# Optimization experiments

Hardware: AMD Instinct MI355X
Metric: run time of the kernel (lower is better)

The kernel has to match this reference:

```python
import jax, jax.numpy as jnp
import numpy as np

DIM = 256
NUM_HEADS = 8
WS = 8
HEAD_DIM = DIM // NUM_HEADS
N = WS * WS
B_NW = 8192


def _relative_position_index():
    coords = np.stack(np.meshgrid(np.arange(WS), np.arange(WS), indexing='ij')).reshape(2, -1)  # [2, N]
    rel = coords[:, :, None] - coords[:, None, :]           # [2, N, N]
    rel = rel.transpose(1, 2, 0)                            # [N, N, 2]
    rel[:, :, 0] += WS - 1
    rel[:, :, 1] += WS - 1
    rel[:, :, 0] *= 2 * WS - 1
    return rel.sum(-1).astype(np.int32)                     # [N, N]


def setup_inputs() -> dict:
    key = jax.random.key(0)
    ks = jax.random.split(key, 6)
    x = jax.random.normal(ks[0], (B_NW, N, DIM), dtype=jnp.float32)
    qkv_w = jax.random.normal(ks[1], (3 * DIM, DIM), dtype=jnp.float32) * (DIM ** -0.5)
    qkv_b = jnp.zeros((3 * DIM,), dtype=jnp.float32)
    proj_w = jax.random.normal(ks[2], (DIM, DIM), dtype=jnp.float32) * (DIM ** -0.5)
    proj_b = jnp.zeros((DIM,), dtype=jnp.float32)
    rel_bias_table = jax.random.normal(ks[3], ((2 * WS - 1) ** 2, NUM_HEADS), dtype=jnp.float32) * 0.02
    rel_pos_index = jnp.asarray(_relative_position_index())
    return {"x": x, "qkv_w": qkv_w, "qkv_b": qkv_b, "proj_w": proj_w,
            "proj_b": proj_b, "rel_bias_table": rel_bias_table,
            "rel_pos_index": rel_pos_index}


def reference(x, qkv_w, qkv_b, proj_w, proj_b, rel_bias_table, rel_pos_index):
    B, Nn, C = x.shape
    scale = HEAD_DIM ** -0.5
    qkv = x @ qkv_w.T + qkv_b                                # [B, N, 3C]
    qkv = qkv.reshape(B, Nn, 3, NUM_HEADS, HEAD_DIM)
    q = qkv[:, :, 0].transpose(0, 2, 1, 3)                   # [B, H, N, d]
    k = qkv[:, :, 1].transpose(0, 2, 1, 3)
    v = qkv[:, :, 2].transpose(0, 2, 1, 3)
    attn = jnp.einsum('bhnd,bhmd->bhnm', q, k) * scale       # [B, H, N, N]
    bias = rel_bias_table[rel_pos_index.reshape(-1)].reshape(Nn, Nn, NUM_HEADS)
    attn = attn + bias.transpose(2, 0, 1)[None]              # add [1, H, N, N]
    attn = jax.nn.softmax(attn, axis=-1)
    out = jnp.einsum('bhnm,bhmd->bhnd', attn, v)             # [B, H, N, d]
    out = out.transpose(0, 2, 1, 3).reshape(B, Nn, C)
    return out @ proj_w.T + proj_b
```

## Files before the change

### kernel.cpp

```cpp
#include <hip/hip_runtime.h>
#include <hip/hip_bf16.h>
#include <stdint.h>


typedef __attribute__((ext_vector_type(8))) short bf16x8;
typedef __attribute__((ext_vector_type(4))) float f32x4;

#define QK_LD 520
#define VT_LD 72
#define X_LD  264
#define SQK_ELEMS (64 * QK_LD)
#define SVT_ELEMS (256 * VT_LD)
#define SX_ELEMS  (64 * X_LD)
#define SMEM_ELEMS (SQK_ELEMS + SVT_ELEMS + SX_ELEMS)
#define SMEM_BYTES (SMEM_ELEMS * 2)

__device__ __forceinline__ unsigned short f2bf(float x) {
  union { __hip_bfloat16 h; unsigned short u; } c;
  c.h = __float2bfloat16(x);
  return c.u;
}
__device__ __forceinline__ float bf2f(unsigned short u) {
  union { unsigned int u; float f; } v; v.u = ((unsigned int)u) << 16;
  return v.f;
}

__global__ void prep_kernel(const float* __restrict__ qkv_w,
                            const float* __restrict__ proj_w,
                            const float* __restrict__ table,
                            const int* __restrict__ idx,
                            unsigned short* __restrict__ wq,
                            unsigned short* __restrict__ wp,
                            unsigned short* __restrict__ bm) {
  int i = blockIdx.x * 256 + threadIdx.x;
  if (i < 196608) {
    wq[i] = f2bf(qkv_w[i]);
  } else if (i < 262144) {
    int j = i - 196608;
    wp[j] = f2bf(proj_w[j]);
  } else {
    int k = i - 262144;
    int h = k >> 12;
    int rc = k & 4095;
    bm[k] = f2bf(table[idx[rc] * 8 + h] * 1.4426950408889634f);
  }
}

__launch_bounds__(1024, 4)
__global__ void lewin_kernel(const float* __restrict__ x,
                             const unsigned short* __restrict__ wq,
                             const float* __restrict__ qkv_b,
                             const unsigned short* __restrict__ wp,
                             const float* __restrict__ proj_b,
                             const unsigned short* __restrict__ bm,
                             float* __restrict__ out) {
  extern __shared__ __align__(16) unsigned short smem[];
  unsigned short* sQK = smem;
  unsigned short* sVT = smem + SQK_ELEMS;
  unsigned short* sX  = sVT + SVT_ELEMS;

  const int b    = blockIdx.x;
  const int tid  = threadIdx.x;
  const int wv   = tid >> 6;
  const int lane = tid & 63;
  const int l16  = lane & 15;
  const int quad = lane >> 4;
  const f32x4 fz = {0.0f, 0.0f, 0.0f, 0.0f};

  const float* xb = x + (size_t)b * 16384;
  #pragma unroll
  for (int it = 0; it < 4; ++it) {
    int f = (it * 1024 + tid) * 4;
    float4 v = *(const float4*)(xb + f);
    int row = f >> 8, col = f & 255;
    ushort4 u;
    u.x = f2bf(v.x); u.y = f2bf(v.y); u.z = f2bf(v.z); u.w = f2bf(v.w);
    *(ushort4*)(sX + row * X_LD + col) = u;
  }
  __syncthreads();

  {
    f32x4 acc[3][4];
    #pragma unroll
    for (int nt = 0; nt < 3; ++nt)
      #pragma unroll
      for (int m = 0; m < 4; ++m) acc[nt][m] = fz;
    const int colb = wv * 48;
    #pragma unroll
    for (int kk = 0; kk < 8; ++kk) {
      bf16x8 a[4];
      #pragma unroll
      for (int m = 0; m < 4; ++m)
        a[m] = *(const bf16x8*)(sX + (16 * m + l16) * X_LD + kk * 32 + quad * 8);
      #pragma unroll
      for (int nt = 0; nt < 3; ++nt) {
        bf16x8 bg = *(const bf16x8*)(wq + (size_t)(colb + nt * 16 + l16) * 256 + kk * 32 + quad * 8);
        #pragma unroll
        for (int m = 0; m < 4; ++m)
          acc[nt][m] = __builtin_amdgcn_mfma_f32_16x16x32_bf16(a[m], bg, acc[nt][m], 0, 0, 0);
      }
    }
    #pragma unroll
    for (int nt = 0; nt < 3; ++nt) {
      int col = colb + nt * 16 + l16;
      float bc = qkv_b[col];
      #pragma unroll
      for (int m = 0; m < 4; ++m) {
        int row0 = 16 * m + quad * 4;
        if (col < 512) {
          #pragma unroll
          for (int r = 0; r < 4; ++r)
            sQK[(row0 + r) * QK_LD + col] = f2bf(acc[nt][m][r] + bc);
        } else {
          int c = col - 512;
          ushort4 u;
          u.x = f2bf(acc[nt][m][0] + bc); u.y = f2bf(acc[nt][m][1] + bc);
          u.z = f2bf(acc[nt][m][2] + bc); u.w = f2bf(acc[nt][m][3] + bc);
          *(ushort4*)(sVT + c * VT_LD + row0) = u;
        }
      }
    }
  }
  __syncthreads();

  const int mt = wv & 3;
  const int hp = wv >> 2;
  unsigned short* sP = sX + hp * 4096;
  const float s2 = 0.17677669529663687f * 1.4426950408889634f;
  f32x4 o[2][2] = {{fz, fz}, {fz, fz}};
  float inv[2][4];

  #pragma unroll
  for (int hh = 0; hh < 2; ++hh) {
    int h = hp * 2 + hh;
    bf16x8 qa = *(const bf16x8*)(sQK + (16 * mt + l16) * QK_LD + h * 32 + quad * 8);
    float e[4][4];
    #pragma unroll
    for (int nt = 0; nt < 4; ++nt) {
      bf16x8 kb = *(const bf16x8*)(sQK + (nt * 16 + l16) * QK_LD + 256 + h * 32 + quad * 8);
      f32x4 a = __builtin_amdgcn_mfma_f32_16x16x32_bf16(qa, kb, fz, 0, 0, 0);
      const unsigned short* bmr = bm + (h * 64 + 16 * mt + quad * 4) * 64 + nt * 16 + l16;
      #pragma unroll
      for (int r = 0; r < 4; ++r)
        e[nt][r] = __builtin_amdgcn_exp2f(fmaf(a[r], s2, bf2f(bmr[r * 64])));
    }
    #pragma unroll
    for (int r = 0; r < 4; ++r) {
      float s = (e[0][r] + e[1][r]) + (e[2][r] + e[3][r]);
      #pragma unroll
      for (int sft = 1; sft < 16; sft <<= 1) s += __shfl_xor(s, sft, 64);
      inv[hh][r] = __builtin_amdgcn_rcpf(s);
      int row = 16 * mt + quad * 4 + r;
      int swz = (row & 7) << 3;
      unsigned short* pd = sP + row * 64;
      pd[(l16 + 0) ^ swz]  = f2bf(e[0][r]);
      pd[(l16 + 16) ^ swz] = f2bf(e[1][r]);
      pd[(l16 + 32) ^ swz] = f2bf(e[2][r]);
      pd[(l16 + 48) ^ swz] = f2bf(e[3][r]);
    }
    int prow = 16 * mt + l16;
    int pswz = (prow & 7) << 3;
    #pragma unroll
    for (int kk = 0; kk < 2; ++kk) {
      bf16x8 pa  = *(const bf16x8*)(sP + prow * 64 + ((kk * 32 + quad * 8) ^ pswz));
      bf16x8 vb0 = *(const bf16x8*)(sVT + (h * 32 + l16) * VT_LD + kk * 32 + quad * 8);
      bf16x8 vb1 = *(const bf16x8*)(sVT + (h * 32 + 16 + l16) * VT_LD + kk * 32 + quad * 8);
      o[hh][0] = __builtin_amdgcn_mfma_f32_16x16x32_bf16(pa, vb0, o[hh][0], 0, 0, 0);
      o[hh][1] = __builtin_amdgcn_mfma_f32_16x16x32_bf16(pa, vb1, o[hh][1], 0, 0, 0);
    }
  }
  __syncthreads();

  unsigned short* sOut = sQK;
  #pragma unroll
  for (int hh = 0; hh < 2; ++hh) {
    int h = hp * 2 + hh;
    #pragma unroll
    for (int r = 0; r < 4; ++r) {
      int orow = 16 * mt + quad * 4 + r;
      sOut[orow * X_LD + h * 32 + l16]      = f2bf(o[hh][0][r] * inv[hh][r]);
      sOut[orow * X_LD + h * 32 + 16 + l16] = f2bf(o[hh][1][r] * inv[hh][r]);
    }
  }
  __syncthreads();

  float* ob = out + (size_t)b * 16384;
  const int col = wv * 16 + l16;
  f32x4 acc[4] = {fz, fz, fz, fz};
  #pragma unroll
  for (int kk = 0; kk < 8; ++kk) {
    bf16x8 bg = *(const bf16x8*)(wp + (size_t)col * 256 + kk * 32 + quad * 8);
    #pragma unroll
    for (int m = 0; m < 4; ++m) {
      bf16x8 a = *(const bf16x8*)(sOut + (16 * m + l16) * X_LD + kk * 32 + quad * 8);
      acc[m] = __builtin_amdgcn_mfma_f32_16x16x32_bf16(a, bg, acc[m], 0, 0, 0);
    }
  }
  float pb = proj_b[col];
  #pragma unroll
  for (int m = 0; m < 4; ++m)
    #pragma unroll
    for (int r = 0; r < 4; ++r)
      ob[(16 * m + quad * 4 + r) * 256 + col] = acc[m][r] + pb;
}

extern "C" void kernel_launch(void* const* d_in, const int* in_sizes, int n_in,
                              void* d_out, int out_size, void* d_ws, size_t ws_size,
                              hipStream_t stream) {
  const float* x      = (const float*)d_in[0];
  const float* qkv_w  = (const float*)d_in[1];
  const float* qkv_b  = (const float*)d_in[2];
  const float* proj_w = (const float*)d_in[3];
  const float* proj_b = (const float*)d_in[4];
  const float* table  = (const float*)d_in[5];
  const int*   idx    = (const int*)d_in[6];
  float* out = (float*)d_out;

  unsigned short* wq = (unsigned short*)d_ws;
  unsigned short* wp = wq + 196608;
  unsigned short* bm = wp + 65536;

  (void)hipFuncSetAttribute((const void*)lewin_kernel,
                            hipFuncAttributeMaxDynamicSharedMemorySize, SMEM_BYTES);

  prep_kernel<<<1152, 256, 0, stream>>>(qkv_w, proj_w, table, idx, wq, wp, bm);
  lewin_kernel<<<8192, 1024, SMEM_BYTES, stream>>>(x, wq, qkv_b, wp, proj_b, bm, out);
}
```

Baseline: 1.416 ms.

## Prefetch weights and bias, compute softmax sums via MFMA, drop a barrier

Issues the x loads, the first QKV weight fragments and the bias-matrix values early, and double-buffers the weight fragments across the k loop, so global-load latency overlaps with compute. Row sums of the softmax are computed with an MFMA against a ones vector instead of shuffle reductions. The normalized attention output is written directly into the dead Q region, which removes one __syncthreads and the separate staging pass. The projection weights are preloaded into registers before attention. The extra live registers (bias values, eight projection weight fragments) raise register pressure under launch bounds of 1024 threads, and sums are now taken over bf16-rounded probabilities.

Result: faster. 1.330 ms (-6.1%).

```diff
diff --git a/kernel.cpp b/kernel.cpp
--- a/kernel.cpp
+++ b/kernel.cpp
@@ -65,16 +65,32 @@
   const int lane = tid & 63;
   const int l16  = lane & 15;
   const int quad = lane >> 4;
+  const int mt   = wv & 3;
+  const int hp   = wv >> 2;
   const f32x4 fz = {0.0f, 0.0f, 0.0f, 0.0f};
 
   const float* xb = x + (size_t)b * 16384;
+  float4 xv[4];
+  #pragma unroll
+  for (int it = 0; it < 4; ++it)
+    xv[it] = *(const float4*)(xb + (size_t)(it * 1024 + tid) * 4);
+
+  const unsigned short* wb2 = wq + (size_t)(wv * 48 + l16) * 256 + quad * 8;
+  bf16x8 bb[2][3];
+  #pragma unroll
+  for (int nt = 0; nt < 3; ++nt)
+    bb[0][nt] = *(const bf16x8*)(wb2 + nt * 4096);
+  float qb[3];
+  #pragma unroll
+  for (int nt = 0; nt < 3; ++nt)
+    qb[nt] = qkv_b[wv * 48 + nt * 16 + l16];
+
   #pragma unroll
   for (int it = 0; it < 4; ++it) {
     int f = (it * 1024 + tid) * 4;
-    float4 v = *(const float4*)(xb + f);
     int row = f >> 8, col = f & 255;
     ushort4 u;
-    u.x = f2bf(v.x); u.y = f2bf(v.y); u.z = f2bf(v.z); u.w = f2bf(v.w);
+    u.x = f2bf(xv[it].x); u.y = f2bf(xv[it].y); u.z = f2bf(xv[it].z); u.w = f2bf(xv[it].w);
     *(ushort4*)(sX + row * X_LD + col) = u;
   }
   __syncthreads();
@@ -85,25 +101,27 @@
     for (int nt = 0; nt < 3; ++nt)
       #pragma unroll
       for (int m = 0; m < 4; ++m) acc[nt][m] = fz;
-    const int colb = wv * 48;
     #pragma unroll
     for (int kk = 0; kk < 8; ++kk) {
+      if (kk < 7) {
+        #pragma unroll
+        for (int nt = 0; nt < 3; ++nt)
+          bb[(kk + 1) & 1][nt] = *(const bf16x8*)(wb2 + nt * 4096 + (kk + 1) * 32);
+      }
       bf16x8 a[4];
       #pragma unroll
       for (int m = 0; m < 4; ++m)
         a[m] = *(const bf16x8*)(sX + (16 * m + l16) * X_LD + kk * 32 + quad * 8);
       #pragma unroll
-      for (int nt = 0; nt < 3; ++nt) {
-        bf16x8 bg = *(const bf16x8*)(wq + (size_t)(colb + nt * 16 + l16) * 256 + kk * 32 + quad * 8);
+      for (int nt = 0; nt < 3; ++nt)
         #pragma unroll
         for (int m = 0; m < 4; ++m)
-          acc[nt][m] = __builtin_amdgcn_mfma_f32_16x16x32_bf16(a[m], bg, acc[nt][m], 0, 0, 0);
-      }
+          acc[nt][m] = __builtin_amdgcn_mfma_f32_16x16x32_bf16(a[m], bb[kk & 1][nt], acc[nt][m], 0, 0, 0);
     }
     #pragma unroll
     for (int nt = 0; nt < 3; ++nt) {
-      int col = colb + nt * 16 + l16;
-      float bc = qkv_b[col];
+      int col = wv * 48 + nt * 16 + l16;
+      float bc = qb[nt];
       #pragma unroll
       for (int m = 0; m < 4; ++m) {
         int row0 = 16 * m + quad * 4;
@@ -121,87 +139,94 @@
       }
     }
   }
+
+  unsigned short bvx[2][4][4];
+  #pragma unroll
+  for (int hh = 0; hh < 2; ++hh) {
+    const unsigned short* bmr0 = bm + ((hp * 2 + hh) * 64 + 16 * mt + quad * 4) * 64 + l16;
+    #pragma unroll
+    for (int nt = 0; nt < 4; ++nt)
+      #pragma unroll
+      for (int r = 0; r < 4; ++r)
+        bvx[hh][nt][r] = bmr0[r * 64 + nt * 16];
+  }
   __syncthreads();
 
-  const int mt = wv & 3;
-  const int hp = wv >> 2;
+  bf16x8 pb4[8];
+  const unsigned short* wr4 = wp + (size_t)(wv * 16 + l16) * 256 + quad * 8;
+  #pragma unroll
+  for (int kk = 0; kk < 8; ++kk)
+    pb4[kk] = *(const bf16x8*)(wr4 + kk * 32);
+  const float pbias = proj_b[wv * 16 + l16];
+
   unsigned short* sP = sX + hp * 4096;
   const float s2 = 0.17677669529663687f * 1.4426950408889634f;
-  f32x4 o[2][2] = {{fz, fz}, {fz, fz}};
-  float inv[2][4];
+  const short onebf = (short)0x3F80;
+  const bf16x8 ones = {onebf, onebf, onebf, onebf, onebf, onebf, onebf, onebf};
+
+  bf16x8 qa0 = *(const bf16x8*)(sQK + (16 * mt + l16) * QK_LD + (hp * 2 + 0) * 32 + quad * 8);
+  bf16x8 qa1 = *(const bf16x8*)(sQK + (16 * mt + l16) * QK_LD + (hp * 2 + 1) * 32 + quad * 8);
 
   #pragma unroll
   for (int hh = 0; hh < 2; ++hh) {
-    int h = hp * 2 + hh;
-    bf16x8 qa = *(const bf16x8*)(sQK + (16 * mt + l16) * QK_LD + h * 32 + quad * 8);
-    float e[4][4];
-    #pragma unroll
-    for (int nt = 0; nt < 4; ++nt) {
-      bf16x8 kb = *(const bf16x8*)(sQK + (nt * 16 + l16) * QK_LD + 256 + h * 32 + quad * 8);
-      f32x4 a = __builtin_amdgcn_mfma_f32_16x16x32_bf16(qa, kb, fz, 0, 0, 0);
-      const unsigned short* bmr = bm + (h * 64 + 16 * mt + quad * 4) * 64 + nt * 16 + l16;
-      #pragma unroll
-      for (int r = 0; r < 4; ++r)
-        e[nt][r] = __builtin_amdgcn_exp2f(fmaf(a[r], s2, bf2f(bmr[r * 64])));
-    }
+    const int h = hp * 2 + hh;
+    const bf16x8 qa = hh ? qa1 : qa0;
+    bf16x8 kb[4];
+    #pragma unroll
+    for (int nt = 0; nt < 4; ++nt)
+      kb[nt] = *(const bf16x8*)(sQK + (nt * 16 + l16) * QK_LD + 256 + h * 32 + quad * 8);
+    f32x4 aq[4];
+    #pragma unroll
+    for (int nt = 0; nt < 4; ++nt)
+      aq[nt] = __builtin_amdgcn_mfma_f32_16x16x32_bf16(qa, kb[nt], fz, 0, 0, 0);
+    #pragma unroll
+    for (int nt = 0; nt < 4; ++nt)
+      #pragma unroll
+      for (int r = 0; r < 4; ++r) {
+        float ev = __builtin_amdgcn_exp2f(fmaf(aq[nt][r], s2, bf2f(bvx[hh][nt][r])));
+        int row = 16 * mt + quad * 4 + r;
+        sP[row * 64 + ((l16 + nt * 16) ^ ((row & 7) << 3))] = f2bf(ev);
+      }
+    const int prow = 16 * mt + l16;
+    const int ps = (l16 & 7) << 3;
+    bf16x8 pa0 = *(const bf16x8*)(sP + prow * 64 + ((quad * 8) ^ ps));
+    bf16x8 pa1 = *(const bf16x8*)(sP + prow * 64 + ((32 + quad * 8) ^ ps));
+    bf16x8 vb00 = *(const bf16x8*)(sVT + (h * 32 + l16) * VT_LD + quad * 8);
+    bf16x8 vb01 = *(const bf16x8*)(sVT + (h * 32 + l16) * VT_LD + 32 + quad * 8);
+    bf16x8 vb10 = *(const bf16x8*)(sVT + (h * 32 + 16 + l16) * VT_LD + quad * 8);
+    bf16x8 vb11 = *(const bf16x8*)(sVT + (h * 32 + 16 + l16) * VT_LD + 32 + quad * 8);
+    f32x4 sa = fz, o0 = fz, o1 = fz;
+    sa = __builtin_amdgcn_mfma_f32_16x16x32_bf16(pa0, ones, sa, 0, 0, 0);
+    sa = __builtin_amdgcn_mfma_f32_16x16x32_bf16(pa1, ones, sa, 0, 0, 0);
+    o0 = __builtin_amdgcn_mfma_f32_16x16x32_bf16(pa0, vb00, o0, 0, 0, 0);
+    o0 = __builtin_amdgcn_mfma_f32_16x16x32_bf16(pa1, vb01, o0, 0, 0, 0);
+    o1 = __builtin_amdgcn_mfma_f32_16x16x32_bf16(pa0, vb10, o1, 0, 0, 0);
+    o1 = __builtin_amdgcn_mfma_f32_16x16x32_bf16(pa1, vb11, o1, 0, 0, 0);
     #pragma unroll
     for (int r = 0; r < 4; ++r) {
-      float s = (e[0][r] + e[1][r]) + (e[2][r] + e[3][r]);
-      #pragma unroll
-      for (int sft = 1; sft < 16; sft <<= 1) s += __shfl_xor(s, sft, 64);
-      inv[hh][r] = __builtin_amdgcn_rcpf(s);
-      int row = 16 * mt + quad * 4 + r;
-      int swz = (row & 7) << 3;
-      unsigned short* pd = sP + row * 64;
-      pd[(l16 + 0) ^ swz]  = f2bf(e[0][r]);
-      pd[(l16 + 16) ^ swz] = f2bf(e[1][r]);
-      pd[(l16 + 32) ^ swz] = f2bf(e[2][r]);
-      pd[(l16 + 48) ^ swz] = f2bf(e[3][r]);
-    }
-    int prow = 16 * mt + l16;
-    int pswz = (prow & 7) << 3;
-    #pragma unroll
-    for (int kk = 0; kk < 2; ++kk) {
-      bf16x8 pa  = *(const bf16x8*)(sP + prow * 64 + ((kk * 32 + quad * 8) ^ pswz));
-      bf16x8 vb0 = *(const bf16x8*)(sVT + (h * 32 + l16) * VT_LD + kk * 32 + quad * 8);
-      bf16x8 vb1 = *(const bf16x8*)(sVT + (h * 32 + 16 + l16) * VT_LD + kk * 32 + quad * 8);
-      o[hh][0] = __builtin_amdgcn_mfma_f32_16x16x32_bf16(pa, vb0, o[hh][0], 0, 0, 0);
-      o[hh][1] = __builtin_amdgcn_mfma_f32_16x16x32_bf16(pa, vb1, o[hh][1], 0, 0, 0);
+      float iv = __builtin_amdgcn_rcpf(sa[r]);
+      int orow = 16 * mt + quad * 4 + r;
+      sQK[orow * QK_LD + h * 32 + l16]      = f2bf(o0[r] * iv);
+      sQK[orow * QK_LD + h * 32 + 16 + l16] = f2bf(o1[r] * iv);
     }
   }
   __syncthreads();
 
-  unsigned short* sOut = sQK;
-  #pragma unroll
-  for (int hh = 0; hh < 2; ++hh) {
-    int h = hp * 2 + hh;
-    #pragma unroll
-    for (int r = 0; r < 4; ++r) {
-      int orow = 16 * mt + quad * 4 + r;
-      sOut[orow * X_LD + h * 32 + l16]      = f2bf(o[hh][0][r] * inv[hh][r]);
-      sOut[orow * X_LD + h * 32 + 16 + l16] = f2bf(o[hh][1][r] * inv[hh][r]);
-    }
-  }
-  __syncthreads();
-
   float* ob = out + (size_t)b * 16384;
-  const int col = wv * 16 + l16;
-  f32x4 acc[4] = {fz, fz, fz, fz};
-  #pragma unroll
-  for (int kk = 0; kk < 8; ++kk) {
-    bf16x8 bg = *(const bf16x8*)(wp + (size_t)col * 256 + kk * 32 + quad * 8);
+  const int col4 = wv * 16 + l16;
+  f32x4 acc4[4] = {fz, fz, fz, fz};
+  #pragma unroll
+  for (int kk = 0; kk < 8; ++kk)
     #pragma unroll
     for (int m = 0; m < 4; ++m) {
-      bf16x8 a = *(const bf16x8*)(sOut + (16 * m + l16) * X_LD + kk * 32 + quad * 8);
-      acc[m] = __builtin_amdgcn_mfma_f32_16x16x32_bf16(a, bg, acc[m], 0, 0, 0);
-    }
-  }
-  float pb = proj_b[col];
+      bf16x8 a = *(const bf16x8*)(sQK + (16 * m + l16) * QK_LD + kk * 32 + quad * 8);
+      acc4[m] = __builtin_amdgcn_mfma_f32_16x16x32_bf16(a, pb4[kk], acc4[m], 0, 0, 0);
+    }
   #pragma unroll
   for (int m = 0; m < 4; ++m)
     #pragma unroll
     for (int r = 0; r < 4; ++r)
-      ob[(16 * m + quad * 4 + r) * 256 + col] = acc[m][r] + pb;
+      ob[(16 * m + quad * 4 + r) * 256 + col4] = acc4[m][r] + pbias;
 }
 
 extern "C" void kernel_launch(void* const* d_in, const int* in_sizes, int n_in,
```
